# Optimization experiments

Hardware: AMD Instinct MI355X
Metric: run time of the kernel (lower is better)

## Reference

```python
import jax, jax.numpy as jnp
import numpy as np

EMBED = 1024
HEADS = 16
HEAD_DIM = EMBED // HEADS


def setup_inputs() -> dict:
    key = jax.random.key(0)
    ks = jax.random.split(key, 11)
    N, S = 2, 2048
    scale = 1.0 / np.sqrt(EMBED)
    inp = {
        "values": jax.random.normal(ks[0], (N, S, EMBED), jnp.float32),
        "keys": jax.random.normal(ks[1], (N, S, EMBED), jnp.float32),
        "queries": jax.random.normal(ks[2], (N, S, EMBED), jnp.float32),
        "W_v": jax.random.normal(ks[3], (EMBED, EMBED), jnp.float32) * scale,
        "b_v": jnp.zeros((EMBED,), jnp.float32),
        "W_k": jax.random.normal(ks[4], (EMBED, EMBED), jnp.float32) * scale,
        "b_k": jnp.zeros((EMBED,), jnp.float32),
        "W_q": jax.random.normal(ks[5], (EMBED, EMBED), jnp.float32) * scale,
        "b_q": jnp.zeros((EMBED,), jnp.float32),
        "W_o": jax.random.normal(ks[6], (EMBED, EMBED), jnp.float32) * scale,
        "b_o": jnp.zeros((EMBED,), jnp.float32),
    }
    return inp


def reference(values, keys, queries, W_v, b_v, W_k, b_k, W_q, b_q, W_o, b_o):
    N, q_len, _ = queries.shape
    # linear projections then split heads: [N, S, H, Dh]
    v = (values @ W_v.T + b_v).reshape(N, -1, HEADS, HEAD_DIM)
    k = (keys @ W_k.T + b_k).reshape(N, -1, HEADS, HEAD_DIM)
    q = (queries @ W_q.T + b_q).reshape(N, q_len, HEADS, HEAD_DIM)
    # raw scores [N, H, Q, K]
    energy = jnp.einsum("nqhd,nkhd->nhqk", q, k)
    attention = jax.nn.softmax(energy / np.sqrt(HEAD_DIM), axis=-1)
    out = jnp.einsum("nhql,nlhd->nqhd", attention, v).reshape(N, q_len, EMBED)
    return out @ W_o.T + b_o
```

## Files before the change

### kernel.cpp

```cpp
#include <hip/hip_runtime.h>
#include <hip/hip_bf16.h>


typedef short bf16x8 __attribute__((ext_vector_type(8)));
typedef short bf16x4 __attribute__((ext_vector_type(4)));
typedef float f32x4 __attribute__((ext_vector_type(4)));

constexpr int S = 2048;
constexpr int E = 1024;
constexpr int H = 16;
constexpr int D = 64;
constexpr int M = 2 * S;
#define QSCALE 0.18033688011112042f

static __device__ __forceinline__ short f2bf_rne(float x) {
  unsigned u = __builtin_bit_cast(unsigned, x);
  u += 0x7fff + ((u >> 16) & 1);
  return (short)(u >> 16);
}
static __device__ __forceinline__ bf16x8 cvt8(float4 a, float4 b) {
  bf16x8 t;
  t[0] = f2bf_rne(a.x); t[1] = f2bf_rne(a.y);
  t[2] = f2bf_rne(a.z); t[3] = f2bf_rne(a.w);
  t[4] = f2bf_rne(b.x); t[5] = f2bf_rne(b.y);
  t[6] = f2bf_rne(b.z); t[7] = f2bf_rne(b.w);
  return t;
}
static __device__ __forceinline__ float fast_exp2(float x) {
#if __has_builtin(__builtin_amdgcn_exp2f)
  return __builtin_amdgcn_exp2f(x);
#else
  return __expf(0.69314718055994531f * x);
#endif
}

static __device__ __forceinline__ void gl_lds16(const short* g, short* l) {
  __builtin_amdgcn_global_load_lds(
      (const __attribute__((address_space(1))) void*)g,
      (__attribute__((address_space(3))) void*)l, 16, 0, 0);
}


__global__ __launch_bounds__(256) void cast_a(
    const float* __restrict__ qs, const float* __restrict__ ks,
    const float* __restrict__ wq, const float* __restrict__ wk,
    const float* __restrict__ wv, const float* __restrict__ wo,
    short* __restrict__ qbf, short* __restrict__ kbf, short* __restrict__ wqb,
    short* __restrict__ wkb, short* __restrict__ wvb, short* __restrict__ wob) {
  const float* s;
  short* d;
  switch (blockIdx.y) {
    case 0: s = qs; d = qbf; break;
    case 1: s = ks; d = kbf; break;
    case 2: if (blockIdx.x >= 512) return; s = wq; d = wqb; break;
    case 3: if (blockIdx.x >= 512) return; s = wk; d = wkb; break;
    case 4: if (blockIdx.x >= 512) return; s = wv; d = wvb; break;
    default: if (blockIdx.x >= 512) return; s = wo; d = wob; break;
  }
  size_t i = ((size_t)blockIdx.x * 256 + threadIdx.x) * 8;
  *(bf16x8*)&d[i] = cvt8(*(const float4*)&s[i], *(const float4*)&s[i + 4]);
}

__global__ __launch_bounds__(256) void cast_one(const float* __restrict__ s,
                                                short* __restrict__ d) {
  size_t i = ((size_t)blockIdx.x * 256 + threadIdx.x) * 8;
  *(bf16x8*)&d[i] = cvt8(*(const float4*)&s[i], *(const float4*)&s[i + 4]);
}

__global__ __launch_bounds__(256) void qk_gemm(
    const short* __restrict__ qbf, const short* __restrict__ kbf,
    const short* __restrict__ wqb, const short* __restrict__ wkb,
    const float* __restrict__ bq, const float* __restrict__ bk,
    short* __restrict__ qb, short* __restrict__ kb) {
  __shared__ __align__(16) short as[128 * 32];
  __shared__ __align__(16) short bs[128 * 32];
  const int tid = threadIdx.x;
  const int lane = tid & 63, w = tid >> 6;
  const int l15 = lane & 15, quad = lane >> 4;
  const int wm = w & 1, wn = w >> 1;

  const int b = blockIdx.x;
  const int c = b & 7, r = b >> 3;
  const int bn = r & 7;
  const int t = c * 8 + (r >> 3);
  const int z = t >> 5, bm = t & 31;

  const short* A = z ? kbf : qbf;
  const short* Bw = z ? wkb : wqb;
  const float* bias = z ? bk : bq;

  const short* agp[2];
  const short* bgp[2];
  int ldsb[2];
#pragma unroll
  for (int cc = 0; cc < 2; ++cc) {
    int seg = w * 2 + cc;
    int p = seg * 8 + (lane >> 3), kc = lane & 7;
    int l = kc ^ (p & 7);
    int row = 2 * p + (l >> 2), col = (l & 3) * 8;
    ldsb[cc] = seg * 512;
    agp[cc] = &A[(size_t)(bm * 128 + row) * E + col];
    bgp[cc] = &Bw[(size_t)(bn * 128 + row) * E + col];
  }

  f32x4 acc[4][4] = {};
  for (int k0 = 0; k0 < E; k0 += 32) {
    __syncthreads();
#pragma unroll
    for (int cc = 0; cc < 2; ++cc) {
      gl_lds16(agp[cc] + k0, &as[ldsb[cc]]);
      gl_lds16(bgp[cc] + k0, &bs[ldsb[cc]]);
    }
    __syncthreads();

    bf16x8 af[4], bf[4];
#pragma unroll
    for (int tt = 0; tt < 4; ++tt) {
      int ra = wm * 64 + tt * 16 + l15;
      int pa2 = ra >> 1, la = (ra & 1) * 4 + quad, ka = la ^ (pa2 & 7);
      af[tt] = *(bf16x8*)&as[pa2 * 64 + ka * 8];
      int rb = wn * 64 + tt * 16 + l15;
      int pb2 = rb >> 1, lb = (rb & 1) * 4 + quad, kb2 = lb ^ (pb2 & 7);
      bf[tt] = *(bf16x8*)&bs[pb2 * 64 + kb2 * 8];
    }
#pragma unroll
    for (int mt = 0; mt < 4; ++mt)
#pragma unroll
      for (int nt = 0; nt < 4; ++nt)
        acc[mt][nt] = __builtin_amdgcn_mfma_f32_16x16x32_bf16(
            af[mt], bf[nt], acc[mt][nt], 0, 0, 0);
  }

#pragma unroll
  for (int mt = 0; mt < 4; ++mt)
#pragma unroll
    for (int nt = 0; nt < 4; ++nt)
#pragma unroll
      for (int rr = 0; rr < 4; ++rr) {
        int row = bm * 128 + wm * 64 + mt * 16 + quad * 4 + rr;
        int col = bn * 128 + wn * 64 + nt * 16 + l15;
        float v = acc[mt][nt][rr] + bias[col];
        int n = row >> 11, s = row & 2047, h = col >> 6, d = col & 63;
        if (z == 0) {
          qb[(((size_t)(n * H + h) * S) + s) * D + d] = f2bf_rne(v * QSCALE);
        } else {
          kb[(((size_t)(n * H + h) * S) + s) * D + d] = f2bf_rne(v);
        }
      }
}

template <int MODE>
__global__ __launch_bounds__(256) void gemm64(const short* __restrict__ A,
                                              const short* __restrict__ Bw,
                                              const float* __restrict__ bias,
                                              void* __restrict__ outp) {
  __shared__ __align__(16) short as[64 * 32];
  __shared__ __align__(16) short bs[128 * 32];
  const int tid = threadIdx.x;
  const int lane = tid & 63, w = tid >> 6;
  const int l15 = lane & 15, quad = lane >> 4;
  const int wm = w & 1, wn = w >> 1;

  const int b = blockIdx.x;
  const int c = b & 7, r = b >> 3;
  const int bn = r & 7;
  const int bm = c * 8 + (r >> 3);

  const short* agp;
  int aldsb;
  {
    int seg = w;
    int p = seg * 8 + (lane >> 3), kc = lane & 7;
    int l = kc ^ (p & 7);
    int row = 2 * p + (l >> 2), col = (l & 3) * 8;
    aldsb = seg * 512;
    agp = &A[(size_t)(bm * 64 + row) * E + col];
  }
  const short* bgp[2];
  int bldsb[2];
#pragma unroll
  for (int cc = 0; cc < 2; ++cc) {
    int seg = w * 2 + cc;
    int p = seg * 8 + (lane >> 3), kc = lane & 7;
    int l = kc ^ (p & 7);
    int row = 2 * p + (l >> 2), col = (l & 3) * 8;
    bldsb[cc] = seg * 512;
    bgp[cc] = &Bw[(size_t)(bn * 128 + row) * E + col];
  }

  f32x4 acc[2][4] = {};
  for (int k0 = 0; k0 < E; k0 += 32) {
    __syncthreads();
    gl_lds16(agp + k0, &as[aldsb]);
#pragma unroll
    for (int cc = 0; cc < 2; ++cc) gl_lds16(bgp[cc] + k0, &bs[bldsb[cc]]);
    __syncthreads();

    bf16x8 af[2], bf[4];
#pragma unroll
    for (int tt = 0; tt < 2; ++tt) {
      int ra = wm * 32 + tt * 16 + l15;
      int pa2 = ra >> 1, la = (ra & 1) * 4 + quad, ka = la ^ (pa2 & 7);
      af[tt] = *(bf16x8*)&as[pa2 * 64 + ka * 8];
    }
#pragma unroll
    for (int tt = 0; tt < 4; ++tt) {
      int rb = wn * 64 + tt * 16 + l15;
      int pb2 = rb >> 1, lb = (rb & 1) * 4 + quad, kb2 = lb ^ (pb2 & 7);
      bf[tt] = *(bf16x8*)&bs[pb2 * 64 + kb2 * 8];
    }
#pragma unroll
    for (int mt = 0; mt < 2; ++mt)
#pragma unroll
      for (int nt = 0; nt < 4; ++nt)
        acc[mt][nt] = __builtin_amdgcn_mfma_f32_16x16x32_bf16(
            af[mt], bf[nt], acc[mt][nt], 0, 0, 0);
  }

#pragma unroll
  for (int mt = 0; mt < 2; ++mt)
#pragma unroll
    for (int nt = 0; nt < 4; ++nt)
#pragma unroll
      for (int rr = 0; rr < 4; ++rr) {
        int row = bm * 64 + wm * 32 + mt * 16 + quad * 4 + rr;
        int col = bn * 128 + wn * 64 + nt * 16 + l15;
        float v = acc[mt][nt][rr] + bias[col];
        if (MODE == 0) {
          int n = row >> 11, s = row & 2047, h = col >> 6, d = col & 63;
          ((short*)outp)[(((size_t)(n * H + h) * D) + d) * S + s] =
              f2bf_rne(v);
        } else {
          ((float*)outp)[(size_t)row * E + col] = v;
        }
      }
}

__global__ __launch_bounds__(512) void attn_kernel(const short* __restrict__ q,
                                                   const short* __restrict__ k,
                                                   const short* __restrict__ vt,
                                                   short* __restrict__ ctx) {
  __shared__ __align__(16) short ks[128 * 72];
  __shared__ __align__(16) short vs[64 * 136];
  __shared__ __align__(16) short ps[8 * 16 * 72];

  const int tid = threadIdx.x;
  const int lane = tid & 63, wv = tid >> 6;
  const int l15 = lane & 15, quad = lane >> 4;

  const int bid = blockIdx.y * gridDim.x + blockIdx.x;
  const int c = bid & 7, r = bid >> 3;
  const int qt = r & 15;
  const int hz = c * 4 + (r >> 4);
  const int hh = hz & 15, nn = hz >> 4;

  const int nh = nn * H + hh;
  const size_t base = (size_t)nh * S * D;
  const int q0 = qt * 128 + wv * 16;
  const int pb = wv * 16 * 72;

  bf16x8 qf[2];
#pragma unroll
  for (int kk = 0; kk < 2; ++kk)
    qf[kk] = *(const bf16x8*)&q[base + (size_t)(q0 + l15) * D +
                                kk * 32 + quad * 8];

  f32x4 o[4] = {};
  float lsum = 0.f;

  bf16x8 pk[2], pv[2];
  auto loadKV = [&](int j0) {
#pragma unroll
    for (int cc = 0; cc < 2; ++cc) {
      int ch = cc * 512 + tid;
      int kr = ch >> 3, kc = (ch & 7) * 8;
      pk[cc] = *(const bf16x8*)&k[base + (size_t)(j0 + kr) * D + kc];
      int vr = ch >> 4, vc = (ch & 15) * 8;
      pv[cc] = *(const bf16x8*)&vt[base + (size_t)vr * S + j0 + vc];
    }
  };

  loadKV(0);
  for (int j0 = 0; j0 < S; j0 += 128) {
    __syncthreads();
#pragma unroll
    for (int cc = 0; cc < 2; ++cc) {
      int ch = cc * 512 + tid;
      int kr = ch >> 3, kc = (ch & 7) * 8;
      *(bf16x8*)&ks[kr * 72 + kc] = pk[cc];
      int vr = ch >> 4, vc = (ch & 15) * 8;
      *(bf16x8*)&vs[vr * 136 + vc] = pv[cc];
    }
    __syncthreads();
    if (j0 + 128 < S) loadKV(j0 + 128);

#pragma unroll
    for (int half = 0; half < 2; ++half) {
      f32x4 sc[4] = {};
#pragma unroll
      for (int kk = 0; kk < 2; ++kk)
#pragma unroll
        for (int kt = 0; kt < 4; ++kt) {
          bf16x8 kf = *(bf16x8*)&ks[(half * 64 + kt * 16 + l15) * 72 +
                                    kk * 32 + quad * 8];
          sc[kt] = __builtin_amdgcn_mfma_f32_16x16x32_bf16(kf, qf[kk], sc[kt],
                                                           0, 0, 0);
        }

#pragma unroll
      for (int kt = 0; kt < 4; ++kt) {
        bf16x4 pq;
#pragma unroll
        for (int rr = 0; rr < 4; ++rr) {
          float p = fast_exp2(sc[kt][rr]);
          lsum += p;
          pq[rr] = f2bf_rne(p);
        }
        *(bf16x4*)&ps[pb + l15 * 72 + kt * 16 + quad * 4] = pq;
      }

#pragma unroll
      for (int kk = 0; kk < 2; ++kk) {
        bf16x8 af = *(bf16x8*)&ps[pb + l15 * 72 + kk * 32 + quad * 8];
#pragma unroll
        for (int nd = 0; nd < 4; ++nd) {
          bf16x8 bfv = *(bf16x8*)&vs[(nd * 16 + l15) * 136 + half * 64 +
                                     kk * 32 + quad * 8];
          o[nd] = __builtin_amdgcn_mfma_f32_16x16x32_bf16(af, bfv, o[nd],
                                                          0, 0, 0);
        }
      }
    }
  }

  lsum += __shfl_xor(lsum, 16);
  lsum += __shfl_xor(lsum, 32);

#pragma unroll
  for (int rr = 0; rr < 4; ++rr) {
    int src = (lane & 48) + ((lane >> 4) & 3) * 4 + rr;
    float lfull = __shfl(lsum, src);
    float inv = 1.0f / lfull;
    int srow = q0 + quad * 4 + rr;
#pragma unroll
    for (int nd = 0; nd < 4; ++nd) {
      int d = nd * 16 + l15;
      ctx[((size_t)(nn * S + srow)) * E + hh * D + d] =
          f2bf_rne(o[nd][rr] * inv);
    }
  }
}

extern "C" void kernel_launch(void* const* d_in, const int* in_sizes, int n_in,
                              void* d_out, int out_size, void* d_ws,
                              size_t ws_size, hipStream_t stream) {
  const float* values  = (const float*)d_in[0];
  const float* keys    = (const float*)d_in[1];
  const float* queries = (const float*)d_in[2];
  const float* b_v = (const float*)d_in[4];
  const float* b_k = (const float*)d_in[6];
  const float* b_q = (const float*)d_in[8];
  const float* W_v = (const float*)d_in[3];
  const float* W_k = (const float*)d_in[5];
  const float* W_q = (const float*)d_in[7];
  const float* W_o = (const float*)d_in[9];
  const float* b_o = (const float*)d_in[10];

  const size_t X = (size_t)M * E;
  const size_t W = (size_t)E * E;

  short* qb  = (short*)d_out;
  short* qbf = (short*)d_out + X;
  short* kb      = (short*)d_ws;
  short* vtb     = kb + X;
  short* castbuf = vtb + X;
  short* wqb = castbuf + X;
  short* wkb = wqb + W;
  short* wvb = wkb + W;
  short* wob = wvb + W;
  short* kbf = castbuf;
  short* vbf = castbuf;
  short* ctx = castbuf;

  cast_a<<<dim3(2048, 6), 256, 0, stream>>>(queries, keys, W_q, W_k, W_v, W_o,
                                            qbf, kbf, wqb, wkb, wvb, wob);
  qk_gemm<<<512, 256, 0, stream>>>(qbf, kbf, wqb, wkb, b_q, b_k, qb, kb);
  cast_one<<<2048, 256, 0, stream>>>(values, vbf);
  gemm64<0><<<512, 256, 0, stream>>>(vbf, wvb, b_v, vtb);
  attn_kernel<<<dim3(16, 32), 512, 0, stream>>>(qb, kb, vtb, ctx);
  gemm64<1><<<512, 256, 0, stream>>>(ctx, wob, b_o, d_out);
}
```

Baseline: 233.0 us.

## Use 32x32x16 MFMA in attention and keep P in registers via permlane swap

The attention kernel moves from 16x16x32 to 32x32x16 bf16 MFMA, so each wave handles 32 query rows and each block 256 rows, halving the grid. The softmax probabilities are packed with v_cvt_pk_bf16_f32 and rearranged with v_permlane32_swap into the A-operand layout, which removes the LDS round trip through the ps buffer. This halves the number of blocks, so K/V tiles are loaded into LDS half as many times in total. The cost is higher register pressure and fewer blocks (256) to spread across the CUs.

```diff
diff --git a/kernel.cpp b/kernel.cpp
--- a/kernel.cpp
+++ b/kernel.cpp
@@ -5,6 +5,9 @@
 typedef short bf16x8 __attribute__((ext_vector_type(8)));
 typedef short bf16x4 __attribute__((ext_vector_type(4)));
 typedef float f32x4 __attribute__((ext_vector_type(4)));
+typedef float f32x16 __attribute__((ext_vector_type(16)));
+typedef unsigned u32x2 __attribute__((ext_vector_type(2)));
+typedef unsigned u32x4 __attribute__((ext_vector_type(4)));
 
 constexpr int S = 2048;
 constexpr int E = 1024;
@@ -31,6 +34,19 @@
   return __builtin_amdgcn_exp2f(x);
 #else
   return __expf(0.69314718055994531f * x);
+#endif
+}
+static __device__ __forceinline__ unsigned cvtpk(float a, float b) {
+  unsigned r;
+  asm("v_cvt_pk_bf16_f32 %0, %1, %2" : "=v"(r) : "v"(a), "v"(b));
+  return r;
+}
+static __device__ __forceinline__ void plswap(unsigned& a, unsigned& b) {
+#if __has_builtin(__builtin_amdgcn_permlane32_swap)
+  u32x2 t = __builtin_amdgcn_permlane32_swap(a, b, false, false);
+  a = t[0]; b = t[1];
+#else
+  asm("v_permlane32_swap_b32 %0, %1" : "+v"(a), "+v"(b));
 #endif
 }
 
@@ -242,30 +258,26 @@
                                                    short* __restrict__ ctx) {
   __shared__ __align__(16) short ks[128 * 72];
   __shared__ __align__(16) short vs[64 * 136];
-  __shared__ __align__(16) short ps[8 * 16 * 72];
 
   const int tid = threadIdx.x;
   const int lane = tid & 63, wv = tid >> 6;
-  const int l15 = lane & 15, quad = lane >> 4;
+  const int l31 = lane & 31, h = lane >> 5;
 
   const int bid = blockIdx.y * gridDim.x + blockIdx.x;
   const int c = bid & 7, r = bid >> 3;
-  const int qt = r & 15;
-  const int hz = c * 4 + (r >> 4);
+  const int qt = r & 7;
+  const int hz = c * 4 + (r >> 3);
   const int hh = hz & 15, nn = hz >> 4;
 
-  const int nh = nn * H + hh;
-  const size_t base = (size_t)nh * S * D;
-  const int q0 = qt * 128 + wv * 16;
-  const int pb = wv * 16 * 72;
-
-  bf16x8 qf[2];
-#pragma unroll
-  for (int kk = 0; kk < 2; ++kk)
-    qf[kk] = *(const bf16x8*)&q[base + (size_t)(q0 + l15) * D +
-                                kk * 32 + quad * 8];
-
-  f32x4 o[4] = {};
+  const size_t base = (size_t)(nn * H + hh) * S * D;
+  const int q0 = qt * 256 + wv * 32;
+
+  bf16x8 qf[4];
+#pragma unroll
+  for (int kd = 0; kd < 4; ++kd)
+    qf[kd] = *(const bf16x8*)&q[base + (size_t)(q0 + l31) * D + kd * 16 + h * 8];
+
+  f32x16 o[2] = {};
   float lsum = 0.f;
 
   bf16x8 pk[2], pv[2];
@@ -296,57 +308,65 @@
 
 #pragma unroll
     for (int half = 0; half < 2; ++half) {
-      f32x4 sc[4] = {};
-#pragma unroll
-      for (int kk = 0; kk < 2; ++kk)
-#pragma unroll
-        for (int kt = 0; kt < 4; ++kt) {
-          bf16x8 kf = *(bf16x8*)&ks[(half * 64 + kt * 16 + l15) * 72 +
-                                    kk * 32 + quad * 8];
-          sc[kt] = __builtin_amdgcn_mfma_f32_16x16x32_bf16(kf, qf[kk], sc[kt],
+      f32x16 sc[2] = {};
+#pragma unroll
+      for (int c2 = 0; c2 < 2; ++c2)
+#pragma unroll
+        for (int kd = 0; kd < 4; ++kd) {
+          bf16x8 kf = *(bf16x8*)&ks[(half * 64 + c2 * 32 + l31) * 72 +
+                                    kd * 16 + h * 8];
+          sc[c2] = __builtin_amdgcn_mfma_f32_32x32x16_bf16(kf, qf[kd], sc[c2],
                                                            0, 0, 0);
         }
 
-#pragma unroll
-      for (int kt = 0; kt < 4; ++kt) {
-        bf16x4 pq;
-#pragma unroll
-        for (int rr = 0; rr < 4; ++rr) {
-          float p = fast_exp2(sc[kt][rr]);
+      bf16x8 pa[4];
+#pragma unroll
+      for (int c2 = 0; c2 < 2; ++c2) {
+        float pe[16];
+#pragma unroll
+        for (int rr = 0; rr < 16; ++rr) {
+          float p = fast_exp2(sc[c2][rr]);
           lsum += p;
-          pq[rr] = f2bf_rne(p);
-        }
-        *(bf16x4*)&ps[pb + l15 * 72 + kt * 16 + quad * 4] = pq;
+          pe[rr] = p;
+        }
+#pragma unroll
+        for (int kk = 0; kk < 2; ++kk) {
+          unsigned A0 = cvtpk(pe[8 * kk + 0], pe[8 * kk + 1]);
+          unsigned A1 = cvtpk(pe[8 * kk + 2], pe[8 * kk + 3]);
+          unsigned B0 = cvtpk(pe[8 * kk + 4], pe[8 * kk + 5]);
+          unsigned B1 = cvtpk(pe[8 * kk + 6], pe[8 * kk + 7]);
+          plswap(A0, B0);
+          plswap(A1, B1);
+          u32x4 t;
+          t[0] = A0; t[1] = A1; t[2] = B0; t[3] = B1;
+          pa[c2 * 2 + kk] = __builtin_bit_cast(bf16x8, t);
+        }
       }
 
 #pragma unroll
-      for (int kk = 0; kk < 2; ++kk) {
-        bf16x8 af = *(bf16x8*)&ps[pb + l15 * 72 + kk * 32 + quad * 8];
-#pragma unroll
-        for (int nd = 0; nd < 4; ++nd) {
-          bf16x8 bfv = *(bf16x8*)&vs[(nd * 16 + l15) * 136 + half * 64 +
-                                     kk * 32 + quad * 8];
-          o[nd] = __builtin_amdgcn_mfma_f32_16x16x32_bf16(af, bfv, o[nd],
+      for (int ks2 = 0; ks2 < 4; ++ks2)
+#pragma unroll
+        for (int dc = 0; dc < 2; ++dc) {
+          bf16x8 vf = *(bf16x8*)&vs[(dc * 32 + l31) * 136 + half * 64 +
+                                    ks2 * 16 + h * 8];
+          o[dc] = __builtin_amdgcn_mfma_f32_32x32x16_bf16(pa[ks2], vf, o[dc],
                                                           0, 0, 0);
         }
-      }
-    }
-  }
-
-  lsum += __shfl_xor(lsum, 16);
+    }
+  }
+
   lsum += __shfl_xor(lsum, 32);
-
-#pragma unroll
-  for (int rr = 0; rr < 4; ++rr) {
-    int src = (lane & 48) + ((lane >> 4) & 3) * 4 + rr;
-    float lfull = __shfl(lsum, src);
-    float inv = 1.0f / lfull;
-    int srow = q0 + quad * 4 + rr;
-#pragma unroll
-    for (int nd = 0; nd < 4; ++nd) {
-      int d = nd * 16 + l15;
-      ctx[((size_t)(nn * S + srow)) * E + hh * D + d] =
-          f2bf_rne(o[nd][rr] * inv);
+  float invq = 1.0f / lsum;
+
+#pragma unroll
+  for (int rr = 0; rr < 16; ++rr) {
+    int crow = (rr & 3) + 8 * (rr >> 2) + 4 * h;
+    float inv = __shfl(invq, crow);
+    int row = q0 + crow;
+#pragma unroll
+    for (int dc = 0; dc < 2; ++dc) {
+      ctx[((size_t)(nn * S + row)) * E + hh * D + dc * 32 + l31] =
+          f2bf_rne(o[dc][rr] * inv);
     }
   }
 }
@@ -387,6 +407,6 @@
   qk_gemm<<<512, 256, 0, stream>>>(qbf, kbf, wqb, wkb, b_q, b_k, qb, kb);
   cast_one<<<2048, 256, 0, stream>>>(values, vbf);
   gemm64<0><<<512, 256, 0, stream>>>(vbf, wvb, b_v, vtb);
-  attn_kernel<<<dim3(16, 32), 512, 0, stream>>>(qb, kb, vtb, ctx);
+  attn_kernel<<<dim3(8, 32), 512, 0, stream>>>(qb, kb, vtb, ctx);
   gemm64<1><<<512, 256, 0, stream>>>(ctx, wob, b_o, d_out);
 }
```

After: 217.9 us. -6.5%, faster.
